# Kernel tuning notes

Hardware: AMD Instinct MI355X
Metric: run time of the kernel (lower is better)

The kernel has to match this reference:

```python
import jax, jax.numpy as jnp
import numpy as np
from jax import lax

B, H, W, CL, CC, CD, NH, NP = 8, 48, 48, 384, 384, 384, 12, 4
N = H * W
HD = CL // NH
SCALE = HD ** -0.5


def _pool_mat(n, out=7):
    # torch AdaptiveAvgPool2d bin edges: [floor(i*n/out), ceil((i+1)*n/out))
    M = np.zeros((out, n), np.float32)
    for i in range(out):
        s = (i * n) // out
        e = -(-((i + 1) * n) // out)
        M[i, s:e] = 1.0 / (e - s)
    return jnp.asarray(M)


def _resize_mat(out_n, in_n):
    # bilinear, align_corners=False (torch F.interpolate)
    M = np.zeros((out_n, in_n), np.float32)
    scale = in_n / out_n
    for o in range(out_n):
        src = (o + 0.5) * scale - 0.5
        src = min(max(src, 0.0), in_n - 1.0)
        i0 = int(np.floor(src))
        i1 = min(i0 + 1, in_n - 1)
        f = src - i0
        M[o, i0] += 1.0 - f
        M[o, i1] += f
    return jnp.asarray(M)


def _ln_c(x, g, b):
    # LayerNorm over channel dim of NCHW, eps=1e-6
    mu = jnp.mean(x, axis=1, keepdims=True)
    var = jnp.mean((x - mu) ** 2, axis=1, keepdims=True)
    xn = (x - mu) * lax.rsqrt(var + 1e-6)
    return xn * g[None, :, None, None] + b[None, :, None, None]


def _c1(x, w):
    # 1x1 conv, w: (out,in)
    return jnp.einsum('oc,bchw->bohw', w, x)


def _bilerp(feat, grid):
    # feat (G,C,Hs,Ws), grid (G,M,2) xy in [-1,1]; align_corners=False, zero padding
    G, C, Hs, Ws = feat.shape
    x = (grid[..., 0] + 1.0) * 0.5 * Ws - 0.5
    y = (grid[..., 1] + 1.0) * 0.5 * Hs - 0.5
    x0 = jnp.floor(x)
    y0 = jnp.floor(y)
    fx = x - x0
    fy = y - y0
    featf = feat.transpose(0, 2, 3, 1).reshape(G, Hs * Ws, C)
    x0i = x0.astype(jnp.int32)
    y0i = y0.astype(jnp.int32)

    def corner(ix, iy):
        valid = ((ix >= 0) & (ix < Ws) & (iy >= 0) & (iy < Hs)).astype(feat.dtype)
        flat = jnp.clip(iy, 0, Hs - 1) * Ws + jnp.clip(ix, 0, Ws - 1)
        g = jax.vmap(lambda f, i: f[i])(featf, flat)  # (G,M,C)
        return g * valid[..., None]

    v00 = corner(x0i, y0i)
    v01 = corner(x0i + 1, y0i)
    v10 = corner(x0i, y0i + 1)
    v11 = corner(x0i + 1, y0i + 1)
    w00 = ((1 - fx) * (1 - fy))[..., None]
    w01 = (fx * (1 - fy))[..., None]
    w10 = ((1 - fx) * fy)[..., None]
    w11 = (fx * fy)[..., None]
    return v00 * w00 + v01 * w01 + v10 * w10 + v11 * w11  # (G,M,C)


def _forward(local_feat, context_prior, deformable_x, W_q, W_k, W_v, W_pre, ln1_g, ln1_b,
             W_post, dw_w, dw_b, ln2_g, ln2_b, W_lo, b_lo, W_off, b_off,
             attention_biases, W_p, bn_g, bn_b, bn_mean, bn_var):
    q = _c1(local_feat, W_q)  # (B,CL,H,W)

    # context_offset_guide: 1x1 -> GELU -> adaptive pool 7x7 -> LN(C) -> 1x1 to 32 -> resize
    cg = jax.nn.gelu(_c1(context_prior, W_pre), approximate=False)
    Mh, Mw = _pool_mat(H), _pool_mat(W)
    pooled = jnp.einsum('oh,pw,bchw->bcop', Mh, Mw, cg)
    guide = _c1(_ln_c(pooled, ln1_g, ln1_b), W_post)  # (B,32,7,7)
    Uh, Uw = _resize_mat(H, 7), _resize_mat(W, 7)
    guide = jnp.einsum('Oh,Pw,bchw->bcOP', Uh, Uw, guide)  # (B,32,H,W)

    # local_offset_base: dwconv3x3 -> LN(C) -> GELU -> 1x1 to 32
    dw = lax.conv_general_dilated(local_feat, dw_w, (1, 1), [(1, 1), (1, 1)],
                                  dimension_numbers=('NCHW', 'OIHW', 'NCHW'),
                                  feature_group_count=CL) + dw_b[None, :, None, None]
    lo = jax.nn.gelu(_ln_c(dw, ln2_g, ln2_b), approximate=False)
    lo = _c1(lo, W_lo) + b_lo[None, :, None, None]  # (B,32,H,W)

    fused = jnp.concatenate([guide, lo], axis=1)  # (B,64,H,W)
    off = _c1(fused, W_off) + b_off[None, :, None, None]  # (B,NH*NP*2,H,W)
    off = off.transpose(0, 2, 3, 1).reshape(B, H, W, NH, NP, 2)
    offn = off / jnp.asarray([W, H], dtype=off.dtype)

    ry = (jnp.arange(H, dtype=off.dtype) + 0.5) / H
    rx = (jnp.arange(W, dtype=off.dtype) + 0.5) / W
    ref = jnp.stack([jnp.broadcast_to(rx[None, :], (H, W)),
                     jnp.broadcast_to(ry[:, None], (H, W))], axis=-1)  # (H,W,2) xy
    grid = (ref[None, :, :, None, None, :] + offn) * 2.0 - 1.0  # (B,H,W,NH,NP,2)

    gridh = grid.reshape(B, N, NH, NP, 2).transpose(0, 2, 1, 3, 4)  # (B,NH,N,NP,2)
    grid_r = gridh.reshape(B * NH, N * NP, 2)

    k = _c1(context_prior, W_k).reshape(B * NH, HD, H, W)
    v = _c1(deformable_x, W_v).reshape(B * NH, HD, H, W)
    k_s = _bilerp(k, grid_r).reshape(B, NH, N, NP, HD)
    v_s = _bilerp(v, grid_r).reshape(B, NH, N, NP, HD)

    qh = q.reshape(B, NH, HD, N).transpose(0, 1, 3, 2)  # (B,NH,N,HD)
    scores = jnp.einsum('bhnd,bhnpd->bhnp', qh, k_s) * SCALE

    # relative position bias: idx(p1,p2) = |dy|*W + |dx| (first-seen enumeration)
    px = jnp.clip(jnp.round((gridh[..., 0] + 1.0) * 0.5 * W - 0.5), 0, W - 1).astype(jnp.int32)
    py = jnp.clip(jnp.round((gridh[..., 1] + 1.0) * 0.5 * H - 0.5), 0, H - 1).astype(jnp.int32)
    n = jnp.arange(N, dtype=jnp.int32)
    qy = (n // W)[None, None, :, None]
    qx = (n % W)[None, None, :, None]
    bidx = jnp.abs(qy - py) * W + jnp.abs(qx - px)  # (B,NH,N,NP)
    bias = attention_biases[jnp.arange(NH)[None, :, None, None], bidx]

    attn = jax.nn.softmax(scores + bias, axis=-1)
    out = jnp.einsum('bhnp,bhnpd->bhnd', attn, v_s)  # (B,NH,N,HD)
    out = out.transpose(0, 1, 3, 2).reshape(B, CL, H, W)

    y = _c1(out, W_p)
    y = bn_g[None, :, None, None] * (y - bn_mean[None, :, None, None]) * \
        lax.rsqrt(bn_var[None, :, None, None] + 1e-5) + bn_b[None, :, None, None]
    return y


def setup_inputs():
    ks = jax.random.split(jax.random.key(0), 16)
    f32 = jnp.float32
    d = {
        'local_feat': jax.random.normal(ks[0], (B, CL, H, W), f32),
        'context_prior': jax.random.normal(ks[1], (B, CC, H, W), f32),
        'deformable_x': jax.random.normal(ks[2], (B, CD, H, W), f32),
        'W_q': jax.random.normal(ks[3], (CL, CL), f32) * 0.02,
        'W_k': jax.random.normal(ks[4], (CL, CC), f32) * 0.02,
        'W_v': jax.random.normal(ks[5], (CD, CD), f32) * 0.02,
        'W_pre': jax.random.normal(ks[6], (CC, CC), f32) * 0.02,
        'ln1_g': jnp.ones((CC,), f32),
        'ln1_b': jnp.zeros((CC,), f32),
        'W_post': jax.random.normal(ks[7], (32, CC), f32) * 0.02,
        'dw_w': jax.random.normal(ks[8], (CL, 1, 3, 3), f32) * 0.1,
        'dw_b': jnp.zeros((CL,), f32),
        'ln2_g': jnp.ones((CL,), f32),
        'ln2_b': jnp.zeros((CL,), f32),
        'W_lo': jax.random.normal(ks[9], (32, CL), f32) * 0.02,
        'b_lo': jnp.zeros((32,), f32),
        'W_off': jax.random.normal(ks[10], (NH * NP * 2, 64), f32) * 0.01,
        'b_off': jax.random.normal(ks[11], (NH * NP * 2,), f32) * 0.5,
        'attention_biases': jax.random.normal(ks[12], (NH, H * W), f32) * 0.02,
        'W_p': jax.random.normal(ks[13], (CL, CL), f32) * 0.02,
        'bn_g': jnp.ones((CL,), f32),
        'bn_b': jnp.zeros((CL,), f32),
        'bn_mean': jax.random.normal(ks[14], (CL,), f32) * 0.01,
        'bn_var': jax.random.uniform(ks[15], (CL,), f32, 0.5, 1.5),
    }
    return d


def reference(local_feat, context_prior, deformable_x, W_q, W_k, W_v, W_pre, ln1_g, ln1_b,
              W_post, dw_w, dw_b, ln2_g, ln2_b, W_lo, b_lo, W_off, b_off,
              attention_biases, W_p, bn_g, bn_b, bn_mean, bn_var):
    return _forward(local_feat, context_prior, deformable_x, W_q, W_k, W_v, W_pre, ln1_g,
                    ln1_b, W_post, dw_w, dw_b, ln2_g, ln2_b, W_lo, b_lo, W_off, b_off,
                    attention_biases, W_p, bn_g, bn_b, bn_mean, bn_var)
```

## Files before the change

kernel.cpp:

```cpp
#include <hip/hip_runtime.h>
#include <hip/hip_bf16.h>
#include <math.h>

#define B_ 8
#define H_ 48
#define W_ 48
#define N_ 2304
#define C_ 384
#define NH_ 12
#define NP_ 4
#define HD_ 32
#define SCALE_ 0.17677669529663687f

typedef unsigned short ushort;
typedef short bf16x8 __attribute__((ext_vector_type(8)));
typedef float f32x4 __attribute__((ext_vector_type(4)));

__device__ __forceinline__ float b2f(ushort u) {
    union { float f; unsigned i; } x; x.i = ((unsigned)u) << 16; return x.f;
}
__device__ __forceinline__ ushort f2b(float f) {
    __hip_bfloat16 h = __float2bfloat16(f);
    return *(ushort*)&h;
}
__device__ __forceinline__ float ldin(const void* p, size_t i, int isbf) {
    return isbf ? b2f(((const ushort*)p)[i]) : ((const float*)p)[i];
}
__device__ __forceinline__ float geluf(float x) {
    return 0.5f * x * (1.0f + erff(x * 0.70710678118654752440f));
}
__device__ __forceinline__ int iabs(int x) { return x < 0 ? -x : x; }

__device__ __forceinline__ void gl_lds16(const ushort* g, ushort* l) {
    __builtin_amdgcn_global_load_lds(
        (const __attribute__((address_space(1))) unsigned int*)g,
        (__attribute__((address_space(3))) unsigned int*)l, 16, 0, 0);
}

enum { EPI_NONE = 0, EPI_GELU = 1, EPI_BN = 3 };

__global__ void probe_kernel(const void* ones_ptr, int* flag) {
    if (threadIdx.x == 0 && blockIdx.x == 0)
        *flag = (*(const unsigned*)ones_ptr == 0x3F803F80u) ? 1 : 0;
}

#define PREP_MAX 24
struct PrepTab {
    const void* src[PREP_MAX];
    void*       dst[PREP_MAX];
    int         n[PREP_MAX];
    int         tobf[PREP_MAX];
};
__global__ __launch_bounds__(256) void prep_kernel(PrepTab tab, int ne, const int* __restrict__ dflag)
{
    const int isbf = *dflag;
    const int e = blockIdx.y;
    if (e >= ne) return;
    const int n = tab.n[e];
    const void* src = tab.src[e];
    if (tab.tobf[e]) {
        ushort* dst = (ushort*)tab.dst[e];
        if (isbf) {
            const ushort* s = (const ushort*)src;
            for (int i = blockIdx.x * 256 + threadIdx.x; i < n; i += gridDim.x * 256)
                dst[i] = s[i];
        } else {
            const float* s = (const float*)src;
            for (int i = blockIdx.x * 256 + threadIdx.x; i < n; i += gridDim.x * 256)
                dst[i] = f2b(s[i]);
        }
    } else {
        float* dst = (float*)tab.dst[e];
        if (isbf) {
            const ushort* s = (const ushort*)src;
            for (int i = blockIdx.x * 256 + threadIdx.x; i < n; i += gridDim.x * 256)
                dst[i] = b2f(s[i]);
        } else {
            const float* s = (const float*)src;
            for (int i = blockIdx.x * 256 + threadIdx.x; i < n; i += gridDim.x * 256)
                dst[i] = s[i];
        }
    }
}

__global__ void dwt_prep_kernel(const float* __restrict__ WdF, float* __restrict__ WdT)
{
    int c = threadIdx.x;
#pragma unroll
    for (int u = 0; u < 9; u++) WdT[u * C_ + c] = WdF[c * 9 + u];
}

struct TPtrs { const void* src[3]; ushort* dst[3]; };
__global__ __launch_bounds__(256) void transpose3_kernel(TPtrs tp, const int* __restrict__ dflag)
{
    const int isbf = *dflag;
    const int which = blockIdx.z >> 3;
    const int b = blockIdx.z & 7;
    const int n0 = blockIdx.x * 64, c0 = blockIdx.y * 32;
    const void* in = tp.src[which];
    ushort* out = tp.dst[which];
    const int t = threadIdx.x;

    __shared__ unsigned tile[64][33];

    if (isbf) {
        {
            const int c = t >> 3, s = t & 7;
            uint4 v = *(const uint4*)((const ushort*)in + ((size_t)b * C_ + c0 + c) * N_ + n0 + s * 8);
            const int nb = s * 8;
            tile[nb + 0][c] = v.x & 0xffff; tile[nb + 1][c] = v.x >> 16;
            tile[nb + 2][c] = v.y & 0xffff; tile[nb + 3][c] = v.y >> 16;
            tile[nb + 4][c] = v.z & 0xffff; tile[nb + 5][c] = v.z >> 16;
            tile[nb + 6][c] = v.w & 0xffff; tile[nb + 7][c] = v.w >> 16;
        }
        __syncthreads();
        {
            const int n = t >> 2, s = t & 3;
            const int cb = s * 8;
            unsigned p0 = tile[n][cb + 0] | (tile[n][cb + 1] << 16);
            unsigned p1 = tile[n][cb + 2] | (tile[n][cb + 3] << 16);
            unsigned p2 = tile[n][cb + 4] | (tile[n][cb + 5] << 16);
            unsigned p3 = tile[n][cb + 6] | (tile[n][cb + 7] << 16);
            uint4 o; o.x = p0; o.y = p1; o.z = p2; o.w = p3;
            *(uint4*)(out + ((size_t)b * N_ + n0 + n) * C_ + c0 + cb) = o;
        }
    } else {
        float* tf = (float*)&tile[0][0];
        const int tx = t & 31, ty = t >> 5;
        for (int sub = 0; sub < 2; sub++) {
            int ns = n0 + sub * 32;
            __syncthreads();
#pragma unroll
            for (int u = 0; u < 4; u++) {
                int c = ty + u * 8;
                tf[c * 33 + tx] = ((const float*)in)[((size_t)b * C_ + c0 + c) * N_ + ns + tx];
            }
            __syncthreads();
#pragma unroll
            for (int u = 0; u < 4; u++) {
                int n = ty + u * 8;
                out[((size_t)b * N_ + ns + n) * C_ + c0 + tx] = f2b(tf[tx * 33 + n]);
            }
        }
    }
}

template <int EPI, int OUTK>
__global__ __launch_bounds__(256) void gemm_mfma(
    const ushort* __restrict__ Ag, const ushort* __restrict__ Bg, void* __restrict__ Yg,
    int M, int NN, int K, size_t a_bs, size_t b_bs,
    const float* __restrict__ p0, const float* __restrict__ p1,
    const float* __restrict__ p2, const float* __restrict__ p3,
    const int* __restrict__ dflag)
{
    const int isbf = (OUTK == 2) ? *dflag : 1;
    __shared__ ushort As[128 * 32];
    __shared__ ushort Bs[128 * 32];
    const int tid = threadIdx.x;
    const int m0 = blockIdx.x * 128;
    const int n0 = blockIdx.y * 128;
    const int b  = blockIdx.z;
    const int lane = tid & 63, wave = tid >> 6;
    const int wr = wave >> 1, wc = wave & 1;
    const int quad = lane >> 4, l15 = lane & 15;

    f32x4 acc[4][4];
#pragma unroll
    for (int i = 0; i < 4; i++)
#pragma unroll
        for (int j = 0; j < 4; j++) acc[i][j] = (f32x4){0.f, 0.f, 0.f, 0.f};

    const size_t abase = (size_t)b * a_bs;
    const size_t bbase = (size_t)b * b_bs;

    for (int kc = 0; kc < K; kc += 32) {
#pragma unroll
        for (int u = 0; u < 2; u++) {
            int idx = tid + 256 * u;
            int r = idx >> 2, s = idx & 3;
            gl_lds16(Ag + abase + (size_t)(m0 + r) * K + kc + 8 * s, &As[idx * 8]);
            gl_lds16(Bg + bbase + (size_t)(n0 + r) * K + kc + 8 * s, &Bs[idx * 8]);
        }
        __syncthreads();
        bf16x8 af[4], bfr[4];
#pragma unroll
        for (int i = 0; i < 4; i++)
            af[i]  = *(const bf16x8*)&As[(wr * 64 + i * 16 + l15) * 32 + quad * 8];
#pragma unroll
        for (int j = 0; j < 4; j++)
            bfr[j] = *(const bf16x8*)&Bs[(wc * 64 + j * 16 + l15) * 32 + quad * 8];
#pragma unroll
        for (int i = 0; i < 4; i++)
#pragma unroll
            for (int j = 0; j < 4; j++)
                acc[i][j] = __builtin_amdgcn_mfma_f32_16x16x32_bf16(af[i], bfr[j], acc[i][j], 0, 0, 0);
        __syncthreads();
    }

    const size_t ybase = (size_t)b * (size_t)M * (size_t)NN;
#pragma unroll
    for (int i = 0; i < 4; i++) {
#pragma unroll
        for (int r = 0; r < 4; r++) {
            int m = m0 + wr * 64 + i * 16 + quad * 4 + r;
            float sc = 1.f, sh = 0.f;
            if (EPI == EPI_BN) {
                sc = p0[m] * rsqrtf(p3[m] + 1e-5f);
                sh = p1[m] - sc * p2[m];
            }
#pragma unroll
            for (int j = 0; j < 4; j++) {
                int nn = n0 + wc * 64 + j * 16 + l15;
                float v = acc[i][j][r];
                if (EPI == EPI_GELU) v = geluf(v);
                if (EPI == EPI_BN) v = sc * v + sh;
                size_t yi = ybase + (size_t)m * NN + nn;
                if (OUTK == 0) ((float*)Yg)[yi] = v;
                else if (OUTK == 1) ((ushort*)Yg)[yi] = f2b(v);
                else { if (isbf) ((ushort*)Yg)[yi] = f2b(v); else ((float*)Yg)[yi] = v; }
            }
        }
    }
}

struct QKVPtrs { const ushort* A[3]; const ushort* Bw[3]; ushort* Y[3]; };
__global__ __launch_bounds__(256) void gemm_qkv_kernel(QKVPtrs qp)
{
    const int which = blockIdx.z >> 3;
    const int b = blockIdx.z & 7;
    const ushort* Ag = qp.A[which];
    const ushort* Bg = qp.Bw[which];
    ushort* Yg = qp.Y[which];

    __shared__ ushort As[128 * 32];
    __shared__ ushort Bs[128 * 32];
    const int tid = threadIdx.x;
    const int m0 = blockIdx.x * 128;
    const int n0 = blockIdx.y * 128;
    const int lane = tid & 63, wave = tid >> 6;
    const int wr = wave >> 1, wc = wave & 1;
    const int quad = lane >> 4, l15 = lane & 15;

    f32x4 acc[4][4];
#pragma unroll
    for (int i = 0; i < 4; i++)
#pragma unroll
        for (int j = 0; j < 4; j++) acc[i][j] = (f32x4){0.f, 0.f, 0.f, 0.f};

    const size_t abase = (size_t)b * (size_t)N_ * C_;

    for (int kc = 0; kc < C_; kc += 32) {
#pragma unroll
        for (int u = 0; u < 2; u++) {
            int idx = tid + 256 * u;
            int r = idx >> 2, s = idx & 3;
            gl_lds16(Ag + abase + (size_t)(m0 + r) * C_ + kc + 8 * s, &As[idx * 8]);
            gl_lds16(Bg + (size_t)(n0 + r) * C_ + kc + 8 * s, &Bs[idx * 8]);
        }
        __syncthreads();
        bf16x8 af[4], bfr[4];
#pragma unroll
        for (int i = 0; i < 4; i++)
            af[i]  = *(const bf16x8*)&As[(wr * 64 + i * 16 + l15) * 32 + quad * 8];
#pragma unroll
        for (int j = 0; j < 4; j++)
            bfr[j] = *(const bf16x8*)&Bs[(wc * 64 + j * 16 + l15) * 32 + quad * 8];
#pragma unroll
        for (int i = 0; i < 4; i++)
#pragma unroll
            for (int j = 0; j < 4; j++)
                acc[i][j] = __builtin_amdgcn_mfma_f32_16x16x32_bf16(af[i], bfr[j], acc[i][j], 0, 0, 0);
        __syncthreads();
    }

    const size_t ybase = abase;
#pragma unroll
    for (int i = 0; i < 4; i++) {
#pragma unroll
        for (int r = 0; r < 4; r++) {
            int m = m0 + wr * 64 + i * 16 + quad * 4 + r;
#pragma unroll
            for (int j = 0; j < 4; j++) {
                int nn = n0 + wc * 64 + j * 16 + l15;
                Yg[ybase + (size_t)m * C_ + nn] = f2b(acc[i][j][r]);
            }
        }
    }
}

__global__ __launch_bounds__(384) void pool_ln_guide_kernel(
    const float* __restrict__ CG, const float* __restrict__ g, const float* __restrict__ bt,
    const ushort* __restrict__ WpostB, float* __restrict__ G7)
{
    const int cell = blockIdx.x % 49, b = blockIdx.x / 49;
    const int i = cell / 7, j = cell % 7, c = threadIdx.x;
    const int sh = (i * H_) / 7, eh = ((i + 1) * H_ + 6) / 7;
    const int sw = (j * W_) / 7, ew = ((j + 1) * W_ + 6) / 7;
    float s = 0.f;
    for (int h = sh; h < eh; h++)
        for (int w = sw; w < ew; w++)
            s += CG[((size_t)b * N_ + h * W_ + w) * C_ + c];
    s *= 1.0f / (float)((eh - sh) * (ew - sw));

    float rs = s, rq = s * s;
#pragma unroll
    for (int m = 1; m <= 32; m <<= 1) {
        rs += __shfl_xor(rs, m);
        rq += __shfl_xor(rq, m);
    }
    __shared__ float ss[6], sq[6], buf[C_];
    __shared__ float psum[12][33];
    int wid = threadIdx.x >> 6;
    if ((threadIdx.x & 63) == 0) { ss[wid] = rs; sq[wid] = rq; }
    __syncthreads();
    if (threadIdx.x == 0) {
        float ts = 0.f, tq = 0.f;
        for (int k = 0; k < 6; k++) { ts += ss[k]; tq += sq[k]; }
        ss[0] = ts; sq[0] = tq;
    }
    __syncthreads();
    float mu = ss[0] / (float)C_;
    float var = sq[0] / (float)C_ - mu * mu;
    float inv = rsqrtf(var + 1e-6f);
    buf[c] = (s - mu) * inv * g[c] + bt[c];
    __syncthreads();

    const int oc = threadIdx.x & 31, seg = threadIdx.x >> 5;
    const uint4* wp = (const uint4*)(WpostB + oc * C_ + seg * 32);
    float part = 0.f;
#pragma unroll
    for (int u = 0; u < 4; u++) {
        uint4 v = wp[u];
        const float* bb = &buf[seg * 32 + u * 8];
        part += b2f((ushort)(v.x & 0xffff)) * bb[0] + b2f((ushort)(v.x >> 16)) * bb[1];
        part += b2f((ushort)(v.y & 0xffff)) * bb[2] + b2f((ushort)(v.y >> 16)) * bb[3];
        part += b2f((ushort)(v.z & 0xffff)) * bb[4] + b2f((ushort)(v.z >> 16)) * bb[5];
        part += b2f((ushort)(v.w & 0xffff)) * bb[6] + b2f((ushort)(v.w >> 16)) * bb[7];
    }
    psum[seg][oc] = part;
    __syncthreads();
    if (threadIdx.x < 32) {
        float acc = 0.f;
#pragma unroll
        for (int k = 0; k < 12; k++) acc += psum[k][threadIdx.x];
        G7[((size_t)b * 49 + cell) * 32 + threadIdx.x] = acc;
    }
}

__global__ __launch_bounds__(384) void wcomb_prep_kernel(
    const ushort* __restrict__ WoffB, const ushort* __restrict__ WloB,
    const float* __restrict__ bloF, const float* __restrict__ boffF,
    ushort* __restrict__ Bext, float* __restrict__ biasp)
{
    const int co = blockIdx.x;
    const int c = threadIdx.x;
    float acc = 0.f;
#pragma unroll 8
    for (int j = 0; j < 32; j++)
        acc += b2f(WoffB[co * 64 + 32 + j]) * b2f(WloB[j * 384 + c]);
    ushort hi = f2b(acc);
    float r = acc - b2f(hi);
    ushort lo = f2b(r);
    Bext[co * 1152 + c] = hi;
    Bext[co * 1152 + 384 + c] = lo;
    Bext[co * 1152 + 768 + c] = hi;
    if (c == 0) {
        float bp = boffF[co];
        for (int j = 0; j < 32; j++)
            bp += b2f(WoffB[co * 64 + 32 + j]) * bloF[j];
        biasp[co] = bp;
    }
}

__global__ void og7_prep_kernel(
    const ushort* __restrict__ WoffB, const float* __restrict__ G7, float* __restrict__ OG7)
{
    const int bc = blockIdx.x;
    const int co = threadIdx.x;
    if (co >= 96) return;
    const float* g = G7 + (size_t)bc * 32;
    float acc = 0.f;
#pragma unroll 8
    for (int c = 0; c < 32; c++)
        acc += b2f(WoffB[co * 64 + c]) * g[c];
    OG7[(size_t)bc * 96 + co] = acc;
}

__global__ __launch_bounds__(512) void dw_ln_gelu_kernel(
    const ushort* __restrict__ LF, const float* __restrict__ WdT, const float* __restrict__ BdF,
    const float* __restrict__ g, const float* __restrict__ bt,
    ushort* __restrict__ AHI, ushort* __restrict__ ALO)
{
    const int wave = threadIdx.x >> 6, lane = threadIdx.x & 63;
    const int m = blockIdx.x * 8 + wave;
    const int b = m / N_, n = m % N_;
    const int h = n / W_, w = n % W_;
    const bool act = lane < 48;
    const int c0 = lane * 8;

    float acc[8];
#pragma unroll
    for (int j = 0; j < 8; j++) acc[j] = 0.f;
    if (act) {
        f32x4 b0 = *(const f32x4*)(BdF + c0);
        f32x4 b1 = *(const f32x4*)(BdF + c0 + 4);
#pragma unroll
        for (int j = 0; j < 4; j++) { acc[j] = b0[j]; acc[4 + j] = b1[j]; }
    }

#pragma unroll
    for (int u = 0; u < 9; u++) {
        const int ky = u / 3, kx = u % 3;
        const int y = h + ky - 1, x = w + kx - 1;
        if (act && y >= 0 && y < H_ && x >= 0 && x < W_) {
            uint4 v = *(const uint4*)(LF + ((size_t)b * N_ + y * W_ + x) * C_ + c0);
            f32x4 wa = *(const f32x4*)(WdT + u * C_ + c0);
            f32x4 wb = *(const f32x4*)(WdT + u * C_ + c0 + 4);
            acc[0] += wa[0] * b2f((ushort)(v.x & 0xffff));
            acc[1] += wa[1] * b2f((ushort)(v.x >> 16));
            acc[2] += wa[2] * b2f((ushort)(v.y & 0xffff));
            acc[3] += wa[3] * b2f((ushort)(v.y >> 16));
            acc[4] += wb[0] * b2f((ushort)(v.z & 0xffff));
            acc[5] += wb[1] * b2f((ushort)(v.z >> 16));
            acc[6] += wb[2] * b2f((ushort)(v.w & 0xffff));
            acc[7] += wb[3] * b2f((ushort)(v.w >> 16));
        }
    }

    float rs = 0.f, rq = 0.f;
#pragma unroll
    for (int j = 0; j < 8; j++) { rs += acc[j]; rq += acc[j] * acc[j]; }
#pragma unroll
    for (int s = 1; s <= 32; s <<= 1) {
        rs += __shfl_xor(rs, s);
        rq += __shfl_xor(rq, s);
    }
    float mu = rs / (float)C_;
    float var = rq / (float)C_ - mu * mu;
    float inv = rsqrtf(var + 1e-6f);

    if (act) {
        f32x4 g0 = *(const f32x4*)(g + c0);
        f32x4 g1 = *(const f32x4*)(g + c0 + 4);
        f32x4 t0 = *(const f32x4*)(bt + c0);
        f32x4 t1 = *(const f32x4*)(bt + c0 + 4);
        float v[8];
#pragma unroll
        for (int j = 0; j < 4; j++) {
            v[j]     = geluf((acc[j]     - mu) * inv * g0[j] + t0[j]);
            v[4 + j] = geluf((acc[4 + j] - mu) * inv * g1[j] + t1[j]);
        }
        uint4 hi, lo;
        ushort hs[8], ls[8];
#pragma unroll
        for (int j = 0; j < 8; j++) {
            hs[j] = f2b(v[j]);
            ls[j] = f2b(v[j] - b2f(hs[j]));
        }
        hi.x = (unsigned)hs[0] | ((unsigned)hs[1] << 16);
        hi.y = (unsigned)hs[2] | ((unsigned)hs[3] << 16);
        hi.z = (unsigned)hs[4] | ((unsigned)hs[5] << 16);
        hi.w = (unsigned)hs[6] | ((unsigned)hs[7] << 16);
        lo.x = (unsigned)ls[0] | ((unsigned)ls[1] << 16);
        lo.y = (unsigned)ls[2] | ((unsigned)ls[3] << 16);
        lo.z = (unsigned)ls[4] | ((unsigned)ls[5] << 16);
        lo.w = (unsigned)ls[6] | ((unsigned)ls[7] << 16);
        size_t idx = (size_t)m * C_ + c0;
        *(uint4*)(AHI + idx) = hi;
        *(uint4*)(ALO + idx) = lo;
    }
}

__global__ __launch_bounds__(256) void off_gemm_kernel(
    const ushort* __restrict__ AHI, const ushort* __restrict__ ALO,
    const ushort* __restrict__ Bext, const float* __restrict__ biasp,
    const float* __restrict__ OG7, float* __restrict__ OFF)
{
    __shared__ short As[128][40];
    __shared__ short Bs[96][40];
    const int tid = threadIdx.x;
    const int m0 = blockIdx.x * 128;
    const int lane = tid & 63, wave = tid >> 6;
    const int wr = wave >> 1, wc = wave & 1;
    const int quad = lane >> 4, l15 = lane & 15;

    f32x4 acc[4][3];
#pragma unroll
    for (int i = 0; i < 4; i++)
#pragma unroll
        for (int j = 0; j < 3; j++) acc[i][j] = (f32x4){0.f, 0.f, 0.f, 0.f};

    for (int kc = 0; kc < 1152; kc += 32) {
        const int seg = kc / 384;
        const int cc0 = kc - seg * 384;
        const ushort* Asrc = (seg < 2) ? AHI : ALO;
#pragma unroll
        for (int u = 0; u < 2; u++) {
            int idx = tid + 256 * u;
            int r = idx >> 2, s = idx & 3;
            *(uint4*)&As[r][s * 8] = *(const uint4*)(Asrc + (size_t)(m0 + r) * 384 + cc0 + 8 * s);
        }
        for (int i = tid; i < 384; i += 256) {
            int r = i >> 2, s = i & 3;
            *(uint4*)&Bs[r][s * 8] = *(const uint4*)(Bext + r * 1152 + kc + 8 * s);
        }
        __syncthreads();
        bf16x8 af[4], bfr[3];
#pragma unroll
        for (int i = 0; i < 4; i++) af[i]  = *(const bf16x8*)&As[wr * 64 + i * 16 + l15][quad * 8];
#pragma unroll
        for (int j = 0; j < 3; j++) bfr[j] = *(const bf16x8*)&Bs[wc * 48 + j * 16 + l15][quad * 8];
#pragma unroll
        for (int i = 0; i < 4; i++)
#pragma unroll
            for (int j = 0; j < 3; j++)
                acc[i][j] = __builtin_amdgcn_mfma_f32_16x16x32_bf16(af[i], bfr[j], acc[i][j], 0, 0, 0);
        __syncthreads();
    }

#pragma unroll
    for (int i = 0; i < 4; i++) {
#pragma unroll
        for (int r = 0; r < 4; r++) {
            int m = m0 + wr * 64 + i * 16 + quad * 4 + r;
            int b = m / N_, n = m - b * N_;
            int Pw = n % W_, Oh = n / W_;
            const float fs = 7.0f / 48.0f;
            float sy = fminf(fmaxf(((float)Oh + 0.5f) * fs - 0.5f, 0.f), 6.f);
            float sx = fminf(fmaxf(((float)Pw + 0.5f) * fs - 0.5f, 0.f), 6.f);
            int y0 = (int)floorf(sy), x0 = (int)floorf(sx);
            int y1 = min(y0 + 1, 6), x1 = min(x0 + 1, 6);
            float fy = sy - (float)y0, fx = sx - (float)x0;
            float w00 = (1.f - fy) * (1.f - fx), w01 = (1.f - fy) * fx;
            float w10 = fy * (1.f - fx), w11 = fy * fx;
            const float* ogb = OG7 + (size_t)b * 49 * 96;
            int c00 = (y0 * 7 + x0) * 96, c01 = (y0 * 7 + x1) * 96;
            int c10 = (y1 * 7 + x0) * 96, c11 = (y1 * 7 + x1) * 96;
#pragma unroll
            for (int j = 0; j < 3; j++) {
                int co = wc * 48 + j * 16 + l15;
                float v = acc[i][j][r] + biasp[co]
                        + w00 * ogb[c00 + co] + w01 * ogb[c01 + co]
                        + w10 * ogb[c10 + co] + w11 * ogb[c11 + co];
                OFF[(size_t)m * 96 + co] = v;
            }
        }
    }
}

__global__ __launch_bounds__(384) void attn_kernel(
    const ushort* __restrict__ Q, const ushort* __restrict__ K, const ushort* __restrict__ V,
    const float* __restrict__ OFF, const float* __restrict__ ABf, ushort* __restrict__ OUT)
{
    const int pairi = blockIdx.x;
    const int b = pairi / (N_ / 2);
    const int n0 = (pairi % (N_ / 2)) * 2;
    const int tid = threadIdx.x;

    __shared__ int   cidxS[96][4];
    __shared__ float cwS[96][4];
    __shared__ float biasS[96];

    if (tid < 96) {
        const int pos = tid / 48, idx = tid % 48;
        const int n = n0 + pos;
        const int h = n / W_, w = n % W_;
        const int nh = idx >> 2, p = idx & 3;
        const size_t ob = ((size_t)b * N_ + n) * 96 + nh * 8 + 2 * p;
        float ox = OFF[ob];
        float oy = OFF[ob + 1];
        float x = (float)w + ox;
        float y = (float)h + oy;

        int px = (int)fminf(fmaxf(rintf(x), 0.f), (float)(W_ - 1));
        int py = (int)fminf(fmaxf(rintf(y), 0.f), (float)(H_ - 1));
        biasS[tid] = ABf[(size_t)nh * N_ + iabs(h - py) * W_ + iabs(w - px)];

        float x0f = floorf(x), y0f = floorf(y);
        float fx = x - x0f, fy = y - y0f;
        int x0 = (int)x0f, y0 = (int)y0f;
#pragma unroll
        for (int cc = 0; cc < 4; cc++) {
            int dx = cc & 1, dy = cc >> 1;
            int ix = x0 + dx, iy = y0 + dy;
            bool valid = (ix >= 0) && (ix < W_) && (iy >= 0) && (iy < H_);
            int ixc = min(max(ix, 0), W_ - 1), iyc = min(max(iy, 0), H_ - 1);
            cidxS[tid][cc] = iyc * W_ + ixc;
            float wx = dx ? fx : (1.f - fx);
            float wy = dy ? fy : (1.f - fy);
            cwS[tid][cc] = valid ? wx * wy : 0.f;
        }
    }
    __syncthreads();

    const int pos = tid / 192, r = tid % 192;
    const int nh = r >> 4, dd = r & 15;
    const int n = n0 + pos;
    const size_t row = ((size_t)b * N_ + n) * C_ + nh * HD_ + dd * 2;
    unsigned qu = *(const unsigned*)(Q + row);
    const float q0 = b2f((ushort)(qu & 0xffff));
    const float q1 = b2f((ushort)(qu >> 16));
    const size_t kvbase = (size_t)b * N_ * C_ + nh * HD_ + dd * 2;
    const int s0 = pos * 48 + nh * 4;

    int   ci[NP_][4];
    float cw[NP_][4];
#pragma unroll
    for (int p = 0; p < NP_; p++)
#pragma unroll
        for (int cc = 0; cc < 4; cc++) {
            ci[p][cc] = cidxS[s0 + p][cc];
            cw[p][cc] = cwS[s0 + p][cc];
        }

    float sc[NP_];
#pragma unroll
    for (int p = 0; p < NP_; p++) {
        float ks0 = 0.f, ks1 = 0.f;
#pragma unroll
        for (int cc = 0; cc < 4; cc++) {
            unsigned kv = *(const unsigned*)(K + kvbase + (size_t)ci[p][cc] * C_);
            ks0 += cw[p][cc] * b2f((ushort)(kv & 0xffff));
            ks1 += cw[p][cc] * b2f((ushort)(kv >> 16));
        }
        float dot = q0 * ks0 + q1 * ks1;
#pragma unroll
        for (int m = 1; m <= 8; m <<= 1) dot += __shfl_xor(dot, m);
        sc[p] = dot * SCALE_ + biasS[s0 + p];
    }

    float m = fmaxf(fmaxf(sc[0], sc[1]), fmaxf(sc[2], sc[3]));
    float e[NP_], esum = 0.f;
#pragma unroll
    for (int p = 0; p < NP_; p++) { e[p] = __expf(sc[p] - m); esum += e[p]; }
    float inv = 1.0f / esum;

    float o0 = 0.f, o1 = 0.f;
#pragma unroll
    for (int p = 0; p < NP_; p++) {
        float vs0 = 0.f, vs1 = 0.f;
#pragma unroll
        for (int cc = 0; cc < 4; cc++) {
            unsigned vv = *(const unsigned*)(V + kvbase + (size_t)ci[p][cc] * C_);
            vs0 += cw[p][cc] * b2f((ushort)(vv & 0xffff));
            vs1 += cw[p][cc] * b2f((ushort)(vv >> 16));
        }
        float ep = e[p] * inv;
        o0 += ep * vs0;
        o1 += ep * vs1;
    }
    unsigned ou = (unsigned)f2b(o0) | ((unsigned)f2b(o1) << 16);
    *(unsigned*)(OUT + row) = ou;
}

extern "C" void kernel_launch(void* const* d_in, const int* in_sizes, int n_in,
                              void* d_out, int out_size, void* d_ws, size_t ws_size,
                              hipStream_t stream)
{
    const void* local_feat    = d_in[0];
    const void* context_prior = d_in[1];
    const void* deformable_x  = d_in[2];

    const size_t BIGE = (size_t)B_ * N_ * C_;

    char* wsb = (char*)d_ws;
    auto carve = [&](size_t bytes) { char* p = wsb; wsb += (bytes + 255) & ~(size_t)255; return p; };
    int*    flag = (int*)carve(256);
    ushort* T1   = (ushort*)carve(BIGE * 2);
    ushort* T2   = (ushort*)carve(BIGE * 2);
    ushort* T3   = (ushort*)carve(BIGE * 2);
    ushort* Qb   = (ushort*)carve(BIGE * 2);
    ushort* Kb   = (ushort*)carve(BIGE * 2);
    float*  CGR  = (float*)carve(BIGE * 4);
    float*  OFFB = (float*)carve((size_t)B_ * N_ * 96 * 4);
    float*  G7   = (float*)carve((size_t)B_ * 49 * 32 * 4);
    ushort* WqB   = (ushort*)carve(147456 * 2);
    ushort* WkB   = (ushort*)carve(147456 * 2);
    ushort* WvB   = (ushort*)carve(147456 * 2);
    ushort* WpreB = (ushort*)carve(147456 * 2);
    ushort* WpB   = (ushort*)carve(147456 * 2);
    ushort* WpostB= (ushort*)carve(12288 * 2);
    ushort* WloB  = (ushort*)carve(12288 * 2);
    ushort* WoffB = (ushort*)carve(6144 * 2);
    ushort* Bext  = (ushort*)carve(96 * 1152 * 2);
    float*  biasp = (float*)carve(96 * 4);
    float*  OG7   = (float*)carve((size_t)B_ * 49 * 96 * 4);
    float*  dwwF  = (float*)carve(3456 * 4);
    float*  dwwT  = (float*)carve(3456 * 4);
    float*  ABf   = (float*)carve(27648 * 4);
    float*  bloF  = (float*)carve(32 * 4);
    float*  boffF = (float*)carve(96 * 4);
    float*  dwbF  = (float*)carve(384 * 4);
    float*  ln1gF = (float*)carve(384 * 4);
    float*  ln1bF = (float*)carve(384 * 4);
    float*  ln2gF = (float*)carve(384 * 4);
    float*  ln2bF = (float*)carve(384 * 4);
    float*  bngF  = (float*)carve(384 * 4);
    float*  bnbF  = (float*)carve(384 * 4);
    float*  bnmF  = (float*)carve(384 * 4);
    float*  bnvF  = (float*)carve(384 * 4);
    ushort* Vb   = (ushort*)CGR;
    ushort* AOut = (ushort*)CGR + BIGE;
    ushort* AHI  = Qb;
    ushort* ALO  = Kb;

    probe_kernel<<<1, 64, 0, stream>>>(d_in[7] , flag);

    PrepTab tab;
    int ne = 0;
    auto add = [&](const void* s, void* d, int n, int tb) {
        tab.src[ne] = s; tab.dst[ne] = d; tab.n[ne] = n; tab.tobf[ne] = tb; ne++;
    };
    add(d_in[3],  WqB,   147456, 1);
    add(d_in[4],  WkB,   147456, 1);
    add(d_in[5],  WvB,   147456, 1);
    add(d_in[6],  WpreB, 147456, 1);
    add(d_in[19], WpB,   147456, 1);
    add(d_in[9],  WpostB, 12288, 1);
    add(d_in[14], WloB,   12288, 1);
    add(d_in[16], WoffB,   6144, 1);
    add(d_in[10], dwwF,    3456, 0);
    add(d_in[18], ABf,    27648, 0);
    add(d_in[15], bloF,      32, 0);
    add(d_in[17], boffF,     96, 0);
    add(d_in[11], dwbF,     384, 0);
    add(d_in[7],  ln1gF,    384, 0);
    add(d_in[8],  ln1bF,    384, 0);
    add(d_in[12], ln2gF,    384, 0);
    add(d_in[13], ln2bF,    384, 0);
    add(d_in[20], bngF,     384, 0);
    add(d_in[21], bnbF,     384, 0);
    add(d_in[22], bnmF,     384, 0);
    add(d_in[23], bnvF,     384, 0);
    prep_kernel<<<dim3(64, ne), 256, 0, stream>>>(tab, ne, flag);
    dwt_prep_kernel<<<1, 384, 0, stream>>>(dwwF, dwwT);

    dim3 blk256(256);
    dim3 t3grid(N_ / 64, C_ / 32, 3 * B_);
    dim3 ggrid(N_ / 128, C_ / 128, B_);
    dim3 qkvgrid(N_ / 128, C_ / 128, 3 * B_);
    dim3 fgrid(C_ / 128, N_ / 128, B_);
    const size_t BST = (size_t)N_ * C_;

    TPtrs tp;
    tp.src[0] = local_feat;    tp.dst[0] = T1;
    tp.src[1] = context_prior; tp.dst[1] = T2;
    tp.src[2] = deformable_x;  tp.dst[2] = T3;
    transpose3_kernel<<<t3grid, blk256, 0, stream>>>(tp, flag);

    wcomb_prep_kernel<<<96, 384, 0, stream>>>(WoffB, WloB, bloF, boffF, Bext, biasp);

    gemm_mfma<EPI_GELU, 0><<<ggrid, blk256, 0, stream>>>(
        T2, WpreB, CGR, N_, C_, C_, BST, 0, nullptr, nullptr, nullptr, nullptr, flag);
    pool_ln_guide_kernel<<<B_ * 49, 384, 0, stream>>>(CGR, ln1gF, ln1bF, WpostB, G7);
    og7_prep_kernel<<<B_ * 49, 96, 0, stream>>>(WoffB, G7, OG7);

    dw_ln_gelu_kernel<<<(B_ * N_) / 8, 512, 0, stream>>>(T1, dwwT, dwbF, ln2gF, ln2bF, AHI, ALO);

    off_gemm_kernel<<<(B_ * N_) / 128, blk256, 0, stream>>>(AHI, ALO, Bext, biasp, OG7, OFFB);

    QKVPtrs qp;
    qp.A[0] = T1; qp.Bw[0] = WqB; qp.Y[0] = Qb;
    qp.A[1] = T2; qp.Bw[1] = WkB; qp.Y[1] = Kb;
    qp.A[2] = T3; qp.Bw[2] = WvB; qp.Y[2] = Vb;
    gemm_qkv_kernel<<<qkvgrid, blk256, 0, stream>>>(qp);

    attn_kernel<<<(B_ * N_) / 2, 384, 0, stream>>>(Qb, Kb, Vb, OFFB, ABf, AOut);

    gemm_mfma<EPI_BN, 2><<<fgrid, blk256, 0, stream>>>(
        WpB, AOut, d_out, C_, N_, C_, 0, BST, bngF, bnbF, bnmF, bnvF, flag);
}
```

Baseline: 383.3 us.

## Multi-stage LDS pipelining for GEMMs and split-K offset GEMM with epilogue moved to attention

The main GEMM kernels and the QKV GEMM now use a 4-buffer LDS ring. They prefetch three K tiles ahead with direct global-to-LDS loads and manual vmcnt waits, and drop the trailing __syncthreads. The offset GEMM is split over its three K segments into a 2D grid writing partial outputs, which raises parallelism. Summing the partials, bias and bilinear guide terms now happens in the attention kernel. This adds workspace and extra reads in attention, and relies on the hand-placed waitcnt/barrier ordering being correct for the ring reuse.

```diff
diff --git a/kernel.cpp b/kernel.cpp
--- a/kernel.cpp
+++ b/kernel.cpp
@@ -22,9 +22,6 @@
 __device__ __forceinline__ ushort f2b(float f) {
     __hip_bfloat16 h = __float2bfloat16(f);
     return *(ushort*)&h;
-}
-__device__ __forceinline__ float ldin(const void* p, size_t i, int isbf) {
-    return isbf ? b2f(((const ushort*)p)[i]) : ((const float*)p)[i];
 }
 __device__ __forceinline__ float geluf(float x) {
     return 0.5f * x * (1.0f + erff(x * 0.70710678118654752440f));
@@ -154,8 +151,8 @@
     const int* __restrict__ dflag)
 {
     const int isbf = (OUTK == 2) ? *dflag : 1;
-    __shared__ ushort As[128 * 32];
-    __shared__ ushort Bs[128 * 32];
+    __shared__ ushort As[4][128 * 32];
+    __shared__ ushort Bs[4][128 * 32];
     const int tid = threadIdx.x;
     const int m0 = blockIdx.x * 128;
     const int n0 = blockIdx.y * 128;
@@ -172,29 +169,42 @@
 
     const size_t abase = (size_t)b * a_bs;
     const size_t bbase = (size_t)b * b_bs;
-
-    for (int kc = 0; kc < K; kc += 32) {
+    const int nt = K / 32;
+
+    auto stage = [&](int p, int kc) {
 #pragma unroll
         for (int u = 0; u < 2; u++) {
             int idx = tid + 256 * u;
             int r = idx >> 2, s = idx & 3;
-            gl_lds16(Ag + abase + (size_t)(m0 + r) * K + kc + 8 * s, &As[idx * 8]);
-            gl_lds16(Bg + bbase + (size_t)(n0 + r) * K + kc + 8 * s, &Bs[idx * 8]);
-        }
-        __syncthreads();
+            gl_lds16(Ag + abase + (size_t)(m0 + r) * K + kc + 8 * s, &As[p][idx * 8]);
+            gl_lds16(Bg + bbase + (size_t)(n0 + r) * K + kc + 8 * s, &Bs[p][idx * 8]);
+        }
+    };
+
+    stage(0, 0);
+    if (nt > 1) stage(1, 32);
+    if (nt > 2) stage(2, 64);
+
+    for (int t = 0; t < nt; ++t) {
+        if (t + 2 < nt)      asm volatile("s_waitcnt vmcnt(8)" ::: "memory");
+        else if (t + 1 < nt) asm volatile("s_waitcnt vmcnt(4)" ::: "memory");
+        else                 asm volatile("s_waitcnt vmcnt(0)" ::: "memory");
+        __builtin_amdgcn_s_barrier();
+        __builtin_amdgcn_sched_barrier(0);
+        if (t + 3 < nt) stage((t + 3) & 3, (t + 3) * 32);
+        const int p = t & 3;
         bf16x8 af[4], bfr[4];
 #pragma unroll
         for (int i = 0; i < 4; i++)
-            af[i]  = *(const bf16x8*)&As[(wr * 64 + i * 16 + l15) * 32 + quad * 8];
+            af[i]  = *(const bf16x8*)&As[p][(wr * 64 + i * 16 + l15) * 32 + quad * 8];
 #pragma unroll
         for (int j = 0; j < 4; j++)
-            bfr[j] = *(const bf16x8*)&Bs[(wc * 64 + j * 16 + l15) * 32 + quad * 8];
+            bfr[j] = *(const bf16x8*)&Bs[p][(wc * 64 + j * 16 + l15) * 32 + quad * 8];
 #pragma unroll
         for (int i = 0; i < 4; i++)
 #pragma unroll
             for (int j = 0; j < 4; j++)
                 acc[i][j] = __builtin_amdgcn_mfma_f32_16x16x32_bf16(af[i], bfr[j], acc[i][j], 0, 0, 0);
-        __syncthreads();
     }
 
     const size_t ybase = (size_t)b * (size_t)M * (size_t)NN;
@@ -232,8 +242,8 @@
     const ushort* Bg = qp.Bw[which];
     ushort* Yg = qp.Y[which];
 
-    __shared__ ushort As[128 * 32];
-    __shared__ ushort Bs[128 * 32];
+    __shared__ ushort As[4][128 * 32];
+    __shared__ ushort Bs[4][128 * 32];
     const int tid = threadIdx.x;
     const int m0 = blockIdx.x * 128;
     const int n0 = blockIdx.y * 128;
@@ -249,28 +259,41 @@
 
     const size_t abase = (size_t)b * (size_t)N_ * C_;
 
-    for (int kc = 0; kc < C_; kc += 32) {
+    auto stage = [&](int p, int kc) {
 #pragma unroll
         for (int u = 0; u < 2; u++) {
             int idx = tid + 256 * u;
             int r = idx >> 2, s = idx & 3;
-            gl_lds16(Ag + abase + (size_t)(m0 + r) * C_ + kc + 8 * s, &As[idx * 8]);
-            gl_lds16(Bg + (size_t)(n0 + r) * C_ + kc + 8 * s, &Bs[idx * 8]);
-        }
-        __syncthreads();
+            gl_lds16(Ag + abase + (size_t)(m0 + r) * C_ + kc + 8 * s, &As[p][idx * 8]);
+            gl_lds16(Bg + (size_t)(n0 + r) * C_ + kc + 8 * s, &Bs[p][idx * 8]);
+        }
+    };
+
+    stage(0, 0);
+    stage(1, 32);
+    stage(2, 64);
+
+    const int nt = C_ / 32;
+    for (int t = 0; t < nt; ++t) {
+        if (t + 2 < nt)      asm volatile("s_waitcnt vmcnt(8)" ::: "memory");
+        else if (t + 1 < nt) asm volatile("s_waitcnt vmcnt(4)" ::: "memory");
+        else                 asm volatile("s_waitcnt vmcnt(0)" ::: "memory");
+        __builtin_amdgcn_s_barrier();
+        __builtin_amdgcn_sched_barrier(0);
+        if (t + 3 < nt) stage((t + 3) & 3, (t + 3) * 32);
+        const int p = t & 3;
         bf16x8 af[4], bfr[4];
 #pragma unroll
         for (int i = 0; i < 4; i++)
-            af[i]  = *(const bf16x8*)&As[(wr * 64 + i * 16 + l15) * 32 + quad * 8];
+            af[i]  = *(const bf16x8*)&As[p][(wr * 64 + i * 16 + l15) * 32 + quad * 8];
 #pragma unroll
         for (int j = 0; j < 4; j++)
-            bfr[j] = *(const bf16x8*)&Bs[(wc * 64 + j * 16 + l15) * 32 + quad * 8];
+            bfr[j] = *(const bf16x8*)&Bs[p][(wc * 64 + j * 16 + l15) * 32 + quad * 8];
 #pragma unroll
         for (int i = 0; i < 4; i++)
 #pragma unroll
             for (int j = 0; j < 4; j++)
                 acc[i][j] = __builtin_amdgcn_mfma_f32_16x16x32_bf16(af[i], bfr[j], acc[i][j], 0, 0, 0);
-        __syncthreads();
     }
 
     const size_t ybase = abase;
@@ -473,13 +496,15 @@
 
 __global__ __launch_bounds__(256) void off_gemm_kernel(
     const ushort* __restrict__ AHI, const ushort* __restrict__ ALO,
-    const ushort* __restrict__ Bext, const float* __restrict__ biasp,
-    const float* __restrict__ OG7, float* __restrict__ OFF)
-{
-    __shared__ short As[128][40];
-    __shared__ short Bs[96][40];
+    const ushort* __restrict__ Bext, float* __restrict__ OFFP)
+{
+    __shared__ ushort As[4][128 * 32];
+    __shared__ ushort Bs[4][128 * 32];
     const int tid = threadIdx.x;
     const int m0 = blockIdx.x * 128;
+    const int seg = blockIdx.y;
+    const ushort* Ag = (seg < 2) ? AHI : ALO;
+    const int bcol0 = seg * 384;
     const int lane = tid & 63, wave = tid >> 6;
     const int wr = wave >> 1, wc = wave & 1;
     const int quad = lane >> 4, l15 = lane & 15;
@@ -490,59 +515,54 @@
 #pragma unroll
         for (int j = 0; j < 3; j++) acc[i][j] = (f32x4){0.f, 0.f, 0.f, 0.f};
 
-    for (int kc = 0; kc < 1152; kc += 32) {
-        const int seg = kc / 384;
-        const int cc0 = kc - seg * 384;
-        const ushort* Asrc = (seg < 2) ? AHI : ALO;
+    auto stage = [&](int p, int kc) {
 #pragma unroll
         for (int u = 0; u < 2; u++) {
             int idx = tid + 256 * u;
             int r = idx >> 2, s = idx & 3;
-            *(uint4*)&As[r][s * 8] = *(const uint4*)(Asrc + (size_t)(m0 + r) * 384 + cc0 + 8 * s);
-        }
-        for (int i = tid; i < 384; i += 256) {
-            int r = i >> 2, s = i & 3;
-            *(uint4*)&Bs[r][s * 8] = *(const uint4*)(Bext + r * 1152 + kc + 8 * s);
-        }
-        __syncthreads();
+            int rb = r < 96 ? r : 95;
+            gl_lds16(Ag + (size_t)(m0 + r) * 384 + kc + 8 * s, &As[p][idx * 8]);
+            gl_lds16(Bext + (size_t)rb * 1152 + bcol0 + kc + 8 * s, &Bs[p][idx * 8]);
+        }
+    };
+
+    stage(0, 0);
+    stage(1, 32);
+    stage(2, 64);
+
+    const int nt = 12;
+    for (int t = 0; t < nt; ++t) {
+        if (t + 2 < nt)      asm volatile("s_waitcnt vmcnt(8)" ::: "memory");
+        else if (t + 1 < nt) asm volatile("s_waitcnt vmcnt(4)" ::: "memory");
+        else                 asm volatile("s_waitcnt vmcnt(0)" ::: "memory");
+        __builtin_amdgcn_s_barrier();
+        __builtin_amdgcn_sched_barrier(0);
+        if (t + 3 < nt) stage((t + 3) & 3, (t + 3) * 32);
+        const int p = t & 3;
         bf16x8 af[4], bfr[3];
 #pragma unroll
-        for (int i = 0; i < 4; i++) af[i]  = *(const bf16x8*)&As[wr * 64 + i * 16 + l15][quad * 8];
-#pragma unroll
-        for (int j = 0; j < 3; j++) bfr[j] = *(const bf16x8*)&Bs[wc * 48 + j * 16 + l15][quad * 8];
+        for (int i = 0; i < 4; i++)
+            af[i]  = *(const bf16x8*)&As[p][(wr * 64 + i * 16 + l15) * 32 + quad * 8];
+#pragma unroll
+        for (int j = 0; j < 3; j++)
+            bfr[j] = *(const bf16x8*)&Bs[p][(wc * 48 + j * 16 + l15) * 32 + quad * 8];
 #pragma unroll
         for (int i = 0; i < 4; i++)
 #pragma unroll
             for (int j = 0; j < 3; j++)
                 acc[i][j] = __builtin_amdgcn_mfma_f32_16x16x32_bf16(af[i], bfr[j], acc[i][j], 0, 0, 0);
-        __syncthreads();
-    }
-
+    }
+
+    float* out = OFFP + (size_t)seg * ((size_t)B_ * N_ * 96);
 #pragma unroll
     for (int i = 0; i < 4; i++) {
 #pragma unroll
         for (int r = 0; r < 4; r++) {
             int m = m0 + wr * 64 + i * 16 + quad * 4 + r;
-            int b = m / N_, n = m - b * N_;
-            int Pw = n % W_, Oh = n / W_;
-            const float fs = 7.0f / 48.0f;
-            float sy = fminf(fmaxf(((float)Oh + 0.5f) * fs - 0.5f, 0.f), 6.f);
-            float sx = fminf(fmaxf(((float)Pw + 0.5f) * fs - 0.5f, 0.f), 6.f);
-            int y0 = (int)floorf(sy), x0 = (int)floorf(sx);
-            int y1 = min(y0 + 1, 6), x1 = min(x0 + 1, 6);
-            float fy = sy - (float)y0, fx = sx - (float)x0;
-            float w00 = (1.f - fy) * (1.f - fx), w01 = (1.f - fy) * fx;
-            float w10 = fy * (1.f - fx), w11 = fy * fx;
-            const float* ogb = OG7 + (size_t)b * 49 * 96;
-            int c00 = (y0 * 7 + x0) * 96, c01 = (y0 * 7 + x1) * 96;
-            int c10 = (y1 * 7 + x0) * 96, c11 = (y1 * 7 + x1) * 96;
 #pragma unroll
             for (int j = 0; j < 3; j++) {
                 int co = wc * 48 + j * 16 + l15;
-                float v = acc[i][j][r] + biasp[co]
-                        + w00 * ogb[c00 + co] + w01 * ogb[c01 + co]
-                        + w10 * ogb[c10 + co] + w11 * ogb[c11 + co];
-                OFF[(size_t)m * 96 + co] = v;
+                out[(size_t)m * 96 + co] = acc[i][j][r];
             }
         }
     }
@@ -550,7 +570,9 @@
 
 __global__ __launch_bounds__(384) void attn_kernel(
     const ushort* __restrict__ Q, const ushort* __restrict__ K, const ushort* __restrict__ V,
-    const float* __restrict__ OFF, const float* __restrict__ ABf, ushort* __restrict__ OUT)
+    const float* __restrict__ OFFP, const float* __restrict__ biasp,
+    const float* __restrict__ OG7,
+    const float* __restrict__ ABf, ushort* __restrict__ OUT)
 {
     const int pairi = blockIdx.x;
     const int b = pairi / (N_ / 2);
@@ -566,9 +588,31 @@
         const int n = n0 + pos;
         const int h = n / W_, w = n % W_;
         const int nh = idx >> 2, p = idx & 3;
-        const size_t ob = ((size_t)b * N_ + n) * 96 + nh * 8 + 2 * p;
-        float ox = OFF[ob];
-        float oy = OFF[ob + 1];
+        const int co = nh * 8 + 2 * p;
+
+        const float fs = 7.0f / 48.0f;
+        float sy = fminf(fmaxf(((float)h + 0.5f) * fs - 0.5f, 0.f), 6.f);
+        float sx = fminf(fmaxf(((float)w + 0.5f) * fs - 0.5f, 0.f), 6.f);
+        int gy0 = (int)floorf(sy), gx0 = (int)floorf(sx);
+        int gy1 = min(gy0 + 1, 6), gx1 = min(gx0 + 1, 6);
+        float gfy = sy - (float)gy0, gfx = sx - (float)gx0;
+        float bw00 = (1.f - gfy) * (1.f - gfx), bw01 = (1.f - gfy) * gfx;
+        float bw10 = gfy * (1.f - gfx), bw11 = gfy * gfx;
+        const float* ogb = OG7 + (size_t)b * 49 * 96;
+        int c00 = (gy0 * 7 + gx0) * 96, c01 = (gy0 * 7 + gx1) * 96;
+        int c10 = (gy1 * 7 + gx0) * 96, c11 = (gy1 * 7 + gx1) * 96;
+        const size_t MS = (size_t)B_ * N_ * 96;
+        const size_t mrow = ((size_t)b * N_ + n) * 96;
+
+        float ox = OFFP[mrow + co] + OFFP[MS + mrow + co] + OFFP[2 * MS + mrow + co]
+                 + biasp[co]
+                 + bw00 * ogb[c00 + co] + bw01 * ogb[c01 + co]
+                 + bw10 * ogb[c10 + co] + bw11 * ogb[c11 + co];
+        float oy = OFFP[mrow + co + 1] + OFFP[MS + mrow + co + 1] + OFFP[2 * MS + mrow + co + 1]
+                 + biasp[co + 1]
+                 + bw00 * ogb[c00 + co + 1] + bw01 * ogb[c01 + co + 1]
+                 + bw10 * ogb[c10 + co + 1] + bw11 * ogb[c11 + co + 1];
+
         float x = (float)w + ox;
         float y = (float)h + oy;
 
@@ -672,7 +716,7 @@
     ushort* Qb   = (ushort*)carve(BIGE * 2);
     ushort* Kb   = (ushort*)carve(BIGE * 2);
     float*  CGR  = (float*)carve(BIGE * 4);
-    float*  OFFB = (float*)carve((size_t)B_ * N_ * 96 * 4);
+    float*  OFFB = (float*)carve((size_t)B_ * N_ * 96 * 4 * 3);
     float*  G7   = (float*)carve((size_t)B_ * 49 * 32 * 4);
     ushort* WqB   = (ushort*)carve(147456 * 2);
     ushort* WkB   = (ushort*)carve(147456 * 2);
@@ -740,6 +784,7 @@
     dim3 ggrid(N_ / 128, C_ / 128, B_);
     dim3 qkvgrid(N_ / 128, C_ / 128, 3 * B_);
     dim3 fgrid(C_ / 128, N_ / 128, B_);
+    dim3 offgrid((B_ * N_) / 128, 3);
     const size_t BST = (size_t)N_ * C_;
 
     TPtrs tp;
@@ -757,7 +802,7 @@
 
     dw_ln_gelu_kernel<<<(B_ * N_) / 8, 512, 0, stream>>>(T1, dwwT, dwbF, ln2gF, ln2bF, AHI, ALO);
 
-    off_gemm_kernel<<<(B_ * N_) / 128, blk256, 0, stream>>>(AHI, ALO, Bext, biasp, OG7, OFFB);
+    off_gemm_kernel<<<offgrid, blk256, 0, stream>>>(AHI, ALO, Bext, OFFB);
 
     QKVPtrs qp;
     qp.A[0] = T1; qp.Bw[0] = WqB; qp.Y[0] = Qb;
@@ -765,7 +810,7 @@
     qp.A[2] = T3; qp.Bw[2] = WvB; qp.Y[2] = Vb;
     gemm_qkv_kernel<<<qkvgrid, blk256, 0, stream>>>(qp);
 
-    attn_kernel<<<(B_ * N_) / 2, 384, 0, stream>>>(Qb, Kb, Vb, OFFB, ABf, AOut);
+    attn_kernel<<<(B_ * N_) / 2, 384, 0, stream>>>(Qb, Kb, Vb, OFFB, biasp, OG7, ABf, AOut);
 
     gemm_mfma<EPI_BN, 2><<<fgrid, blk256, 0, stream>>>(
         WpB, AOut, d_out, C_, N_, C_, 0, BST, bngF, bnbF, bnmF, bnvF, flag);
```

Result: faster. 359.7 us (-6.1%).
